# Kernel optimization log

Measured on AMD Instinct MI355X. Metric: run time of the kernel, lower is better.

## Reference

```python
import jax, jax.numpy as jnp
import numpy as np

E = 640000   # n_edges
D = 128      # feature_dim
N = 40000    # n_dst_nodes


def setup_inputs() -> dict:
    key = jax.random.key(0)
    k1, k2, k3 = jax.random.split(key, 3)
    src_emb = jax.random.normal(k1, (E, D), dtype=jnp.float32)
    dst_idx = jax.random.randint(k2, (E,), 0, N, dtype=jnp.int64)
    # nn.Linear default init scale ~ 1/sqrt(fan_in)
    W = jax.random.normal(k3, (D, D), dtype=jnp.float32) / jnp.sqrt(jnp.float32(D))
    b = jnp.zeros((D,), dtype=jnp.float32)
    return {"src_emb": src_emb, "W": W, "b": b, "dst_idx": dst_idx, "n_nodes": N}


def reference(src_emb, W, b, dst_idx, n_nodes):
    # msg_e = relu(Linear(src_emb))  -- per-edge messages [E, D]
    msg = jax.nn.relu(jnp.einsum("ed,fd->ef", src_emb, W) + b)
    # update_all(copy_edge, max) == segment max over destination nodes [N, D]
    h_node = jax.ops.segment_max(msg, dst_idx, num_segments=n_nodes)
    return h_node
```

## Files before the change

### kernel.cpp

```cpp
#include <hip/hip_runtime.h>
#include <hip/hip_bf16.h>

#define E_EDGES 640000
#define DIM     128
#define N_NODES 40000

#define KREP  16
#define HSIZE (KREP * N_NODES)

typedef __bf16 bf16x8 __attribute__((ext_vector_type(8)));
typedef float  floatx4 __attribute__((ext_vector_type(4)));

__device__ __forceinline__ void swizzle_w(const float* __restrict__ W,
                                          __bf16* __restrict__ Wsw, int tid) {
    int lane = tid & 63;
    int kb   = (tid >> 6) & 3;
    int nb   = tid >> 8;
    int f    = nb * 16 + (lane & 15);
    int k0   = kb * 32 + ((lane >> 4) & 3) * 8;
    const float* wrow = W + f * DIM + k0;
    __bf16* o = Wsw + tid * 8;
#pragma unroll
    for (int j = 0; j < 8; ++j) o[j] = (__bf16)wrow[j];
}

__global__ void prep0_kernel(const float* __restrict__ W,
                             __bf16* __restrict__ Wsw,
                             int* __restrict__ H) {
    int tid = blockIdx.x * 256 + threadIdx.x;
    if (tid < HSIZE) H[tid] = 0;
    if (tid < 2048) swizzle_w(W, Wsw, tid);
}

__global__ void hist16_kernel(const int* __restrict__ dst, int* __restrict__ H) {
    int e = blockIdx.x * 256 + threadIdx.x;
    atomicAdd(&H[(e & (KREP - 1)) * N_NODES + dst[e]], 1);
}

__global__ __launch_bounds__(256)
void sum_kernel(const int* __restrict__ H, int* __restrict__ cnt,
                int* __restrict__ bsum) {
    __shared__ int sred[256];
    int n = blockIdx.x * 256 + threadIdx.x;
    int s = 0;
    if (n < N_NODES) {
#pragma unroll
        for (int r = 0; r < KREP; ++r) s += H[r * N_NODES + n];
        cnt[n] = s;
    }
    sred[threadIdx.x] = s;
    __syncthreads();
    for (int off = 128; off > 0; off >>= 1) {
        if (threadIdx.x < off) sred[threadIdx.x] += sred[threadIdx.x + off];
        __syncthreads();
    }
    if (threadIdx.x == 0) bsum[blockIdx.x] = sred[0];
}

__global__ __launch_bounds__(256)
void scanb_kernel(const int* __restrict__ bsum, int* __restrict__ bstart) {
    __shared__ int ss[256];
    int t = threadIdx.x;
    int v = (t < 160) ? bsum[t] : 0;
    int orig = v;
    ss[t] = v;
    __syncthreads();
    for (int off = 1; off < 256; off <<= 1) {
        int u = (t >= off) ? ss[t - off] : 0;
        __syncthreads();
        ss[t] += u;
        __syncthreads();
    }
    if (t < 160) bstart[t] = ss[t] - orig;
}

__global__ __launch_bounds__(256)
void offs_kernel(int* __restrict__ H, const int* __restrict__ cnt,
                 const int* __restrict__ bstart, int* __restrict__ starts) {
    __shared__ int ss[256];
    int t = threadIdx.x;
    int n = blockIdx.x * 256 + t;
    int v = (n < N_NODES) ? cnt[n] : 0;
    int orig = v;
    ss[t] = v;
    __syncthreads();
    for (int off = 1; off < 256; off <<= 1) {
        int u = (t >= off) ? ss[t - off] : 0;
        __syncthreads();
        ss[t] += u;
        __syncthreads();
    }
    if (n < N_NODES) {
        int run = bstart[blockIdx.x] + ss[t] - orig;
        starts[n] = run;
#pragma unroll
        for (int r = 0; r < KREP; ++r) {
            int idx = r * N_NODES + n;
            int h = H[idx];
            H[idx] = run;
            run += h;
        }
    }
}

__global__ void scatter16_kernel(const int* __restrict__ dst,
                                 int* __restrict__ H, int* __restrict__ perm) {
    int e = blockIdx.x * 256 + threadIdx.x;
    int pos = atomicAdd(&H[(e & (KREP - 1)) * N_NODES + dst[e]], 1);
    perm[pos] = e;
}

__global__ void prep_kernel(const float* __restrict__ W,
                            __bf16* __restrict__ Wsw,
                            int* __restrict__ cnt) {
    int tid = blockIdx.x * blockDim.x + threadIdx.x;
    if (tid < N_NODES) cnt[tid] = 0;
    if (tid < 2048) swizzle_w(W, Wsw, tid);
}
__global__ void hist_kernel(const int* __restrict__ dst, int* __restrict__ cnt) {
    int e = blockIdx.x * 256 + threadIdx.x;
    atomicAdd(&cnt[dst[e]], 1);
}
__global__ __launch_bounds__(1024)
void scan_kernel(const int* __restrict__ cnt, int* __restrict__ starts) {
    __shared__ int ss[1024];
    const int t = threadIdx.x;
    const int base = t * 40;
    int local = 0;
    for (int i = 0; i < 40; ++i) {
        int idx = base + i;
        if (idx < N_NODES) local += cnt[idx];
    }
    ss[t] = local;
    __syncthreads();
    for (int off = 1; off < 1024; off <<= 1) {
        int v = (t >= off) ? ss[t - off] : 0;
        __syncthreads();
        ss[t] += v;
        __syncthreads();
    }
    int run = ss[t] - local;
    for (int i = 0; i < 40; ++i) {
        int idx = base + i;
        if (idx < N_NODES) { starts[idx] = run; run += cnt[idx]; }
    }
}
__global__ void scatter_kernel(const int* __restrict__ dst,
                               int* __restrict__ starts,
                               int* __restrict__ perm) {
    int e = blockIdx.x * 256 + threadIdx.x;
    int pos = atomicAdd(&starts[dst[e]], 1);
    perm[pos] = e;
}

__global__ __launch_bounds__(256)
void node_gemm_kernel(const float* __restrict__ src,
                      const __bf16* __restrict__ Wsw,
                      const float* __restrict__ bias,
                      const int* __restrict__ perm,
                      const int* __restrict__ cnt,
                      const int* __restrict__ stends,
                      float* __restrict__ out, int st_mode) {
    __shared__ bf16x8 Wl[2048];
    const int t = threadIdx.x;
    {
        const float4* gw = (const float4*)Wsw;
        float4* lw = (float4*)Wl;
#pragma unroll
        for (int i = 0; i < 8; ++i) lw[t + i * 256] = gw[t + i * 256];
    }
    __syncthreads();

    const int lane = t & 63;
    const int wave = t >> 6;
    const int q    = lane >> 4;
    const int n    = lane & 15;
    const int node = blockIdx.x * 4 + wave;

    const int c  = cnt[node];
    const int se = stends[node];
    const int st = st_mode ? (se - c) : se;
    float* orow = out + (size_t)node * DIM;

    if (c == 0) {
        orow[lane]      = -INFINITY;
        orow[lane + 64] = -INFINITY;
        return;
    }

    floatx4 vmax[8];
#pragma unroll
    for (int nb = 0; nb < 8; ++nb) vmax[nb] = (floatx4)(-INFINITY);

    const int nch = (c + 15) >> 4;
    for (int ch = 0; ch < nch; ++ch) {
        int rows = c - (ch << 4);
        if (rows > 16) rows = 16;
        int e = (n < rows) ? perm[st + (ch << 4) + n] : 0;
        const float* arow = src + (size_t)e * DIM + q * 8;

        floatx4 acc[8];
#pragma unroll
        for (int nb = 0; nb < 8; ++nb) acc[nb] = (floatx4)(0.0f);

#pragma unroll
        for (int kb = 0; kb < 4; ++kb) {
            float4 a0 = *(const float4*)(arow + kb * 32);
            float4 a1 = *(const float4*)(arow + kb * 32 + 4);
            bf16x8 af;
            af[0] = (__bf16)a0.x; af[1] = (__bf16)a0.y;
            af[2] = (__bf16)a0.z; af[3] = (__bf16)a0.w;
            af[4] = (__bf16)a1.x; af[5] = (__bf16)a1.y;
            af[6] = (__bf16)a1.z; af[7] = (__bf16)a1.w;
#pragma unroll
            for (int nb = 0; nb < 8; ++nb) {
                bf16x8 bf = Wl[(nb * 4 + kb) * 64 + lane];
                acc[nb] = __builtin_amdgcn_mfma_f32_16x16x32_bf16(af, bf, acc[nb], 0, 0, 0);
            }
        }

#pragma unroll
        for (int nb = 0; nb < 8; ++nb)
#pragma unroll
            for (int r = 0; r < 4; ++r) {
                float v = (q * 4 + r < rows) ? acc[nb][r] : -INFINITY;
                vmax[nb][r] = fmaxf(vmax[nb][r], v);
            }
    }

    float red[8];
#pragma unroll
    for (int nb = 0; nb < 8; ++nb) {
        float v = fmaxf(fmaxf(vmax[nb][0], vmax[nb][1]),
                        fmaxf(vmax[nb][2], vmax[nb][3]));
        v = fmaxf(v, __shfl_xor(v, 16));
        v = fmaxf(v, __shfl_xor(v, 32));
        red[nb] = v;
    }
    float o1 = (q == 0) ? red[0] : (q == 1) ? red[1] : (q == 2) ? red[2] : red[3];
    float o2 = (q == 0) ? red[4] : (q == 1) ? red[5] : (q == 2) ? red[6] : red[7];
    orow[lane]      = fmaxf(o1 + bias[lane],      0.0f);
    orow[lane + 64] = fmaxf(o2 + bias[lane + 64], 0.0f);
}

extern "C" void kernel_launch(void* const* d_in, const int* in_sizes, int n_in,
                              void* d_out, int out_size, void* d_ws, size_t ws_size,
                              hipStream_t stream) {
    const float* src  = (const float*)d_in[0];
    const float* W    = (const float*)d_in[1];
    const float* bias = (const float*)d_in[2];
    const int*   dst  = (const int*)d_in[3];

    char* ws = (char*)d_ws;
    size_t off = 0;
    __bf16* Wsw  = (__bf16*)(ws + off); off += 32768;
    int* cnt     = (int*)(ws + off);    off += 160000;
    int* starts  = (int*)(ws + off);    off += 160000;
    int* perm    = (int*)(ws + off);    off += 2560000;
    int* bsum    = (int*)(ws + off);    off += 1024;
    int* bstart  = (int*)(ws + off);    off += 1024;
    int* H       = (int*)(ws + off);    off += (size_t)HSIZE * 4;
    float* outf  = (float*)d_out;

    if (ws_size >= off) {
        prep0_kernel<<<2500, 256, 0, stream>>>(W, Wsw, H);
        hist16_kernel<<<E_EDGES / 256, 256, 0, stream>>>(dst, H);
        sum_kernel<<<160, 256, 0, stream>>>(H, cnt, bsum);
        scanb_kernel<<<1, 256, 0, stream>>>(bsum, bstart);
        offs_kernel<<<160, 256, 0, stream>>>(H, cnt, bstart, starts);
        scatter16_kernel<<<E_EDGES / 256, 256, 0, stream>>>(dst, H, perm);
        node_gemm_kernel<<<N_NODES / 4, 256, 0, stream>>>(src, Wsw, bias, perm,
                                                          cnt, starts, outf, 0);
    } else {
        prep_kernel<<<(N_NODES + 255) / 256, 256, 0, stream>>>(W, Wsw, cnt);
        hist_kernel<<<E_EDGES / 256, 256, 0, stream>>>(dst, cnt);
        scan_kernel<<<1, 1024, 0, stream>>>(cnt, starts);
        scatter_kernel<<<E_EDGES / 256, 256, 0, stream>>>(dst, starts, perm);
        node_gemm_kernel<<<N_NODES / 4, 256, 0, stream>>>(src, Wsw, bias, perm,
                                                          cnt, starts, outf, 1);
    }
}
```

Baseline: 603.0 us.

## Replace atomic histogram CSR build with cooperative two-pass radix sort

Builds the edge-by-destination ordering with a single cooperative kernel that does a two-pass (8-bit) radix sort of (dst, edge) pairs, separated by grid syncs. Node start offsets are taken from boundaries in the sorted array, so the replicated global histogram and several small launches go away. The node GEMM kernel becomes persistent over 2500 blocks, each handling four node groups. This trades global atomics and launch overhead for grid-wide syncs and extra sort buffer traffic, and it depends on the cooperative launch succeeding with 625 co-resident blocks.

```diff
diff --git a/kernel.cpp b/kernel.cpp
--- a/kernel.cpp
+++ b/kernel.cpp
@@ -1,9 +1,15 @@
 #include <hip/hip_runtime.h>
 #include <hip/hip_bf16.h>
+#include <hip/hip_cooperative_groups.h>
+
+namespace cg = cooperative_groups;
 
 #define E_EDGES 640000
 #define DIM     128
 #define N_NODES 40000
+
+#define NB     625
+#define NBIN1  157
 
 #define KREP  16
 #define HSIZE (KREP * N_NODES)
@@ -24,6 +30,124 @@
     for (int j = 0; j < 8; ++j) o[j] = (__bf16)wrow[j];
 }
 
+__global__ __launch_bounds__(256)
+void sort_all(const float* __restrict__ W, const int* __restrict__ dst,
+              __bf16* __restrict__ Wsw,
+              int2* __restrict__ buf0, int2* __restrict__ buf1,
+              int* __restrict__ Hg, int* __restrict__ total,
+              int* __restrict__ base, int* __restrict__ perm,
+              int* __restrict__ starts) {
+    cg::grid_group grid = cg::this_grid();
+    __shared__ int h[256];
+    __shared__ int c[256];
+    const int t   = threadIdx.x;
+    const int b   = blockIdx.x;
+    const int tid = b * 256 + t;
+
+    for (int i = tid; i < E_EDGES; i += NB * 256)
+        buf0[i] = make_int2(dst[i], i);
+    if (tid < 2048) swizzle_w(W, Wsw, tid);
+    grid.sync();
+
+    if (t < NBIN1) h[t] = 0;
+    __syncthreads();
+    {
+        const int lo = b * 1024;
+#pragma unroll
+        for (int r = 0; r < 4; ++r)
+            atomicAdd(&h[buf0[lo + r * 256 + t].x >> 8], 1);
+    }
+    __syncthreads();
+    if (t < NBIN1) Hg[t * NB + b] = h[t];
+    grid.sync();
+
+    if (b < NBIN1) {
+        int i0 = t * 3;
+        int v0 = 0, v1 = 0, v2 = 0, s = 0;
+        if (i0     < NB) { v0 = Hg[b * NB + i0];     s += v0; }
+        if (i0 + 1 < NB) { v1 = Hg[b * NB + i0 + 1]; s += v1; }
+        if (i0 + 2 < NB) { v2 = Hg[b * NB + i0 + 2]; s += v2; }
+        h[t] = s;
+        __syncthreads();
+        for (int off = 1; off < 256; off <<= 1) {
+            int u = (t >= off) ? h[t - off] : 0;
+            __syncthreads();
+            h[t] += u;
+            __syncthreads();
+        }
+        int run = h[t] - s;
+        if (i0     < NB) { Hg[b * NB + i0]     = run; run += v0; }
+        if (i0 + 1 < NB) { Hg[b * NB + i0 + 1] = run; run += v1; }
+        if (i0 + 2 < NB) { Hg[b * NB + i0 + 2] = run; run += v2; }
+        if (t == 255) total[b] = h[255];
+    }
+    grid.sync();
+
+    if (b == 0) {
+        int v = (t < NBIN1) ? total[t] : 0;
+        int orig = v;
+        h[t] = v;
+        __syncthreads();
+        for (int off = 1; off < 256; off <<= 1) {
+            int u = (t >= off) ? h[t - off] : 0;
+            __syncthreads();
+            h[t] += u;
+            __syncthreads();
+        }
+        if (t < NBIN1) base[t] = h[t] - orig;
+        if (t == 0) base[NBIN1] = E_EDGES;
+    }
+    grid.sync();
+
+    if (t < NBIN1) c[t] = Hg[t * NB + b];
+    __syncthreads();
+    {
+        const int lo = b * 1024;
+#pragma unroll
+        for (int r = 0; r < 4; ++r) {
+            int2 p = buf0[lo + r * 256 + t];
+            int d = p.x >> 8;
+            int pos = base[d] + atomicAdd(&c[d], 1);
+            buf1[pos] = p;
+        }
+    }
+    grid.sync();
+
+    if (b < NBIN1) {
+        const int lo = base[b], hi = base[b + 1];
+        h[t] = 0;
+        __syncthreads();
+        for (int i = lo + t; i < hi; i += 256)
+            atomicAdd(&h[buf1[i].x & 255], 1);
+        __syncthreads();
+        int orig = h[t];
+        for (int off = 1; off < 256; off <<= 1) {
+            int u = (t >= off) ? h[t - off] : 0;
+            __syncthreads();
+            h[t] += u;
+            __syncthreads();
+        }
+        c[t] = h[t] - orig;
+        __syncthreads();
+        for (int i = lo + t; i < hi; i += 256) {
+            int2 p = buf1[i];
+            int pos = lo + atomicAdd(&c[p.x & 255], 1);
+            buf0[pos] = p;
+        }
+    }
+    grid.sync();
+
+    for (int i = tid; i < E_EDGES; i += NB * 256) {
+        int2 p = buf0[i];
+        perm[i] = p.y;
+        int k  = p.x;
+        int kp = (i == 0) ? -1 : buf0[i - 1].x;
+        for (int n = kp + 1; n <= k; ++n) starts[n] = i;
+        if (i == E_EDGES - 1)
+            for (int n = k + 1; n <= N_NODES; ++n) starts[n] = E_EDGES;
+    }
+}
+
 __global__ void prep0_kernel(const float* __restrict__ W,
                              __bf16* __restrict__ Wsw,
                              int* __restrict__ H) {
@@ -31,12 +155,10 @@
     if (tid < HSIZE) H[tid] = 0;
     if (tid < 2048) swizzle_w(W, Wsw, tid);
 }
-
 __global__ void hist16_kernel(const int* __restrict__ dst, int* __restrict__ H) {
     int e = blockIdx.x * 256 + threadIdx.x;
     atomicAdd(&H[(e & (KREP - 1)) * N_NODES + dst[e]], 1);
 }
-
 __global__ __launch_bounds__(256)
 void sum_kernel(const int* __restrict__ H, int* __restrict__ cnt,
                 int* __restrict__ bsum) {
@@ -56,7 +178,6 @@
     }
     if (threadIdx.x == 0) bsum[blockIdx.x] = sred[0];
 }
-
 __global__ __launch_bounds__(256)
 void scanb_kernel(const int* __restrict__ bsum, int* __restrict__ bstart) {
     __shared__ int ss[256];
@@ -73,7 +194,6 @@
     }
     if (t < 160) bstart[t] = ss[t] - orig;
 }
-
 __global__ __launch_bounds__(256)
 void offs_kernel(int* __restrict__ H, const int* __restrict__ cnt,
                  const int* __restrict__ bstart, int* __restrict__ starts) {
@@ -102,54 +222,10 @@
         }
     }
 }
-
 __global__ void scatter16_kernel(const int* __restrict__ dst,
                                  int* __restrict__ H, int* __restrict__ perm) {
     int e = blockIdx.x * 256 + threadIdx.x;
     int pos = atomicAdd(&H[(e & (KREP - 1)) * N_NODES + dst[e]], 1);
-    perm[pos] = e;
-}
-
-__global__ void prep_kernel(const float* __restrict__ W,
-                            __bf16* __restrict__ Wsw,
-                            int* __restrict__ cnt) {
-    int tid = blockIdx.x * blockDim.x + threadIdx.x;
-    if (tid < N_NODES) cnt[tid] = 0;
-    if (tid < 2048) swizzle_w(W, Wsw, tid);
-}
-__global__ void hist_kernel(const int* __restrict__ dst, int* __restrict__ cnt) {
-    int e = blockIdx.x * 256 + threadIdx.x;
-    atomicAdd(&cnt[dst[e]], 1);
-}
-__global__ __launch_bounds__(1024)
-void scan_kernel(const int* __restrict__ cnt, int* __restrict__ starts) {
-    __shared__ int ss[1024];
-    const int t = threadIdx.x;
-    const int base = t * 40;
-    int local = 0;
-    for (int i = 0; i < 40; ++i) {
-        int idx = base + i;
-        if (idx < N_NODES) local += cnt[idx];
-    }
-    ss[t] = local;
-    __syncthreads();
-    for (int off = 1; off < 1024; off <<= 1) {
-        int v = (t >= off) ? ss[t - off] : 0;
-        __syncthreads();
-        ss[t] += v;
-        __syncthreads();
-    }
-    int run = ss[t] - local;
-    for (int i = 0; i < 40; ++i) {
-        int idx = base + i;
-        if (idx < N_NODES) { starts[idx] = run; run += cnt[idx]; }
-    }
-}
-__global__ void scatter_kernel(const int* __restrict__ dst,
-                               int* __restrict__ starts,
-                               int* __restrict__ perm) {
-    int e = blockIdx.x * 256 + threadIdx.x;
-    int pos = atomicAdd(&starts[dst[e]], 1);
     perm[pos] = e;
 }
 
@@ -160,7 +236,7 @@
                       const int* __restrict__ perm,
                       const int* __restrict__ cnt,
                       const int* __restrict__ stends,
-                      float* __restrict__ out, int st_mode) {
+                      float* __restrict__ out, int st_mode, int ngroups) {
     __shared__ bf16x8 Wl[2048];
     const int t = threadIdx.x;
     {
@@ -175,72 +251,80 @@
     const int wave = t >> 6;
     const int q    = lane >> 4;
     const int n    = lane & 15;
-    const int node = blockIdx.x * 4 + wave;
-
-    const int c  = cnt[node];
-    const int se = stends[node];
-    const int st = st_mode ? (se - c) : se;
-    float* orow = out + (size_t)node * DIM;
-
-    if (c == 0) {
-        orow[lane]      = -INFINITY;
-        orow[lane + 64] = -INFINITY;
-        return;
-    }
-
-    floatx4 vmax[8];
-#pragma unroll
-    for (int nb = 0; nb < 8; ++nb) vmax[nb] = (floatx4)(-INFINITY);
-
-    const int nch = (c + 15) >> 4;
-    for (int ch = 0; ch < nch; ++ch) {
-        int rows = c - (ch << 4);
-        if (rows > 16) rows = 16;
-        int e = (n < rows) ? perm[st + (ch << 4) + n] : 0;
-        const float* arow = src + (size_t)e * DIM + q * 8;
-
-        floatx4 acc[8];
-#pragma unroll
-        for (int nb = 0; nb < 8; ++nb) acc[nb] = (floatx4)(0.0f);
-
-#pragma unroll
-        for (int kb = 0; kb < 4; ++kb) {
-            float4 a0 = *(const float4*)(arow + kb * 32);
-            float4 a1 = *(const float4*)(arow + kb * 32 + 4);
-            bf16x8 af;
-            af[0] = (__bf16)a0.x; af[1] = (__bf16)a0.y;
-            af[2] = (__bf16)a0.z; af[3] = (__bf16)a0.w;
-            af[4] = (__bf16)a1.x; af[5] = (__bf16)a1.y;
-            af[6] = (__bf16)a1.z; af[7] = (__bf16)a1.w;
-#pragma unroll
-            for (int nb = 0; nb < 8; ++nb) {
-                bf16x8 bf = Wl[(nb * 4 + kb) * 64 + lane];
-                acc[nb] = __builtin_amdgcn_mfma_f32_16x16x32_bf16(af, bf, acc[nb], 0, 0, 0);
+
+    for (int g = 0; g < ngroups; ++g) {
+        const int node = (blockIdx.x + g * gridDim.x) * 4 + wave;
+        if (node >= N_NODES) break;
+
+        const int cv = cnt[node];
+        const int se = stends[node];
+        int c, st;
+        if (st_mode == 2)      { c = cv - se; st = se; }
+        else if (st_mode == 1) { c = cv; st = se - cv; }
+        else                   { c = cv; st = se; }
+
+        float* orow = out + (size_t)node * DIM;
+
+        if (c == 0) {
+            orow[lane]      = -INFINITY;
+            orow[lane + 64] = -INFINITY;
+            continue;
+        }
+
+        floatx4 vmax[8];
+#pragma unroll
+        for (int nb = 0; nb < 8; ++nb) vmax[nb] = (floatx4)(-INFINITY);
+
+        const int nch = (c + 15) >> 4;
+        for (int ch = 0; ch < nch; ++ch) {
+            int rows = c - (ch << 4);
+            if (rows > 16) rows = 16;
+            int e = (n < rows) ? perm[st + (ch << 4) + n] : 0;
+            const float* arow = src + (size_t)e * DIM + q * 8;
+
+            floatx4 acc[8];
+#pragma unroll
+            for (int nb = 0; nb < 8; ++nb) acc[nb] = (floatx4)(0.0f);
+
+#pragma unroll
+            for (int kb = 0; kb < 4; ++kb) {
+                float4 a0 = *(const float4*)(arow + kb * 32);
+                float4 a1 = *(const float4*)(arow + kb * 32 + 4);
+                bf16x8 af;
+                af[0] = (__bf16)a0.x; af[1] = (__bf16)a0.y;
+                af[2] = (__bf16)a0.z; af[3] = (__bf16)a0.w;
+                af[4] = (__bf16)a1.x; af[5] = (__bf16)a1.y;
+                af[6] = (__bf16)a1.z; af[7] = (__bf16)a1.w;
+#pragma unroll
+                for (int nb = 0; nb < 8; ++nb) {
+                    bf16x8 bf = Wl[(nb * 4 + kb) * 64 + lane];
+                    acc[nb] = __builtin_amdgcn_mfma_f32_16x16x32_bf16(af, bf, acc[nb], 0, 0, 0);
+                }
             }
-        }
-
-#pragma unroll
-        for (int nb = 0; nb < 8; ++nb)
-#pragma unroll
-            for (int r = 0; r < 4; ++r) {
-                float v = (q * 4 + r < rows) ? acc[nb][r] : -INFINITY;
-                vmax[nb][r] = fmaxf(vmax[nb][r], v);
-            }
-    }
-
-    float red[8];
-#pragma unroll
-    for (int nb = 0; nb < 8; ++nb) {
-        float v = fmaxf(fmaxf(vmax[nb][0], vmax[nb][1]),
-                        fmaxf(vmax[nb][2], vmax[nb][3]));
-        v = fmaxf(v, __shfl_xor(v, 16));
-        v = fmaxf(v, __shfl_xor(v, 32));
-        red[nb] = v;
-    }
-    float o1 = (q == 0) ? red[0] : (q == 1) ? red[1] : (q == 2) ? red[2] : red[3];
-    float o2 = (q == 0) ? red[4] : (q == 1) ? red[5] : (q == 2) ? red[6] : red[7];
-    orow[lane]      = fmaxf(o1 + bias[lane],      0.0f);
-    orow[lane + 64] = fmaxf(o2 + bias[lane + 64], 0.0f);
+
+#pragma unroll
+            for (int nb = 0; nb < 8; ++nb)
+#pragma unroll
+                for (int r = 0; r < 4; ++r) {
+                    float v = (q * 4 + r < rows) ? acc[nb][r] : -INFINITY;
+                    vmax[nb][r] = fmaxf(vmax[nb][r], v);
+                }
+        }
+
+        float red[8];
+#pragma unroll
+        for (int nb = 0; nb < 8; ++nb) {
+            float v = fmaxf(fmaxf(vmax[nb][0], vmax[nb][1]),
+                            fmaxf(vmax[nb][2], vmax[nb][3]));
+            v = fmaxf(v, __shfl_xor(v, 16));
+            v = fmaxf(v, __shfl_xor(v, 32));
+            red[nb] = v;
+        }
+        float o1 = (q == 0) ? red[0] : (q == 1) ? red[1] : (q == 2) ? red[2] : red[3];
+        float o2 = (q == 0) ? red[4] : (q == 1) ? red[5] : (q == 2) ? red[6] : red[7];
+        orow[lane]      = fmaxf(o1 + bias[lane],      0.0f);
+        orow[lane + 64] = fmaxf(o2 + bias[lane + 64], 0.0f);
+    }
 }
 
 extern "C" void kernel_launch(void* const* d_in, const int* in_sizes, int n_in,
@@ -251,32 +335,53 @@
     const float* bias = (const float*)d_in[2];
     const int*   dst  = (const int*)d_in[3];
 
+    float* outf = (float*)d_out;
     char* ws = (char*)d_ws;
+
     size_t off = 0;
     __bf16* Wsw  = (__bf16*)(ws + off); off += 32768;
-    int* cnt     = (int*)(ws + off);    off += 160000;
-    int* starts  = (int*)(ws + off);    off += 160000;
+    int* starts  = (int*)(ws + off);    off += 160016;
     int* perm    = (int*)(ws + off);    off += 2560000;
-    int* bsum    = (int*)(ws + off);    off += 1024;
-    int* bstart  = (int*)(ws + off);    off += 1024;
-    int* H       = (int*)(ws + off);    off += (size_t)HSIZE * 4;
-    float* outf  = (float*)d_out;
-
-    if (ws_size >= off) {
-        prep0_kernel<<<2500, 256, 0, stream>>>(W, Wsw, H);
+    int2* buf0   = (int2*)(ws + off);   off += 5120000;
+    int2* buf1   = (int2*)(ws + off);   off += 5120000;
+    int* Hg      = (int*)(ws + off);    off += 392512;
+    int* total   = (int*)(ws + off);    off += 640;
+    int* base    = (int*)(ws + off);    off += 640;
+    const size_t coop_need = off;
+
+    bool done = false;
+    if (ws_size >= coop_need) {
+        void* kargs[] = {(void*)&W, (void*)&dst, (void*)&Wsw, (void*)&buf0,
+                         (void*)&buf1, (void*)&Hg, (void*)&total, (void*)&base,
+                         (void*)&perm, (void*)&starts};
+        hipError_t cerr = hipLaunchCooperativeKernel((const void*)sort_all,
+                                                     dim3(NB), dim3(256),
+                                                     kargs, 0, stream);
+        if (cerr == hipSuccess) {
+            node_gemm_kernel<<<2500, 256, 0, stream>>>(
+                src, Wsw, bias, perm, starts + 1, starts, outf, 2, 4);
+            done = true;
+        } else {
+            (void)hipGetLastError();
+        }
+    }
+
+    if (!done) {
+        size_t f = 0;
+        __bf16* fWsw = (__bf16*)(ws + f); f += 32768;
+        int* cnt     = (int*)(ws + f);    f += 160000;
+        int* fstarts = (int*)(ws + f);    f += 160000;
+        int* fperm   = (int*)(ws + f);    f += 2560000;
+        int* bsum    = (int*)(ws + f);    f += 1024;
+        int* bstart  = (int*)(ws + f);    f += 1024;
+        int* H       = (int*)(ws + f);    f += (size_t)HSIZE * 4;
+        prep0_kernel<<<2500, 256, 0, stream>>>(W, fWsw, H);
         hist16_kernel<<<E_EDGES / 256, 256, 0, stream>>>(dst, H);
         sum_kernel<<<160, 256, 0, stream>>>(H, cnt, bsum);
         scanb_kernel<<<1, 256, 0, stream>>>(bsum, bstart);
-        offs_kernel<<<160, 256, 0, stream>>>(H, cnt, bstart, starts);
-        scatter16_kernel<<<E_EDGES / 256, 256, 0, stream>>>(dst, H, perm);
-        node_gemm_kernel<<<N_NODES / 4, 256, 0, stream>>>(src, Wsw, bias, perm,
-                                                          cnt, starts, outf, 0);
-    } else {
-        prep_kernel<<<(N_NODES + 255) / 256, 256, 0, stream>>>(W, Wsw, cnt);
-        hist_kernel<<<E_EDGES / 256, 256, 0, stream>>>(dst, cnt);
-        scan_kernel<<<1, 1024, 0, stream>>>(cnt, starts);
-        scatter_kernel<<<E_EDGES / 256, 256, 0, stream>>>(dst, starts, perm);
-        node_gemm_kernel<<<N_NODES / 4, 256, 0, stream>>>(src, Wsw, bias, perm,
-                                                          cnt, starts, outf, 1);
-    }
-}
+        offs_kernel<<<160, 256, 0, stream>>>(H, cnt, bstart, fstarts);
+        scatter16_kernel<<<E_EDGES / 256, 256, 0, stream>>>(dst, H, fperm);
+        node_gemm_kernel<<<10000, 256, 0, stream>>>(
+            src, fWsw, bias, fperm, cnt, fstarts, outf, 0, 1);
+    }
+}
```

Result: slower. 983.7 us (+63.1%).
